# Performance work log

Hardware: AMD Instinct MI355X
Metric: run time of the kernel (lower is better)

Reference implementation:

```python
import jax, jax.numpy as jnp
import numpy as np

N_NODES = 100_000
N_EDGES = 3_200_000
D_IN, D_EDGE, D_HID, D_OUT = 8, 4, 32, 16
NEG_SLOPE = 0.2  # PyG GATv2Conv default


def setup_inputs() -> dict:
    key = jax.random.key(0)
    ks = jax.random.split(key, 13)
    s = 0.1
    return {
        "x": jax.random.normal(ks[0], (N_NODES, D_IN), jnp.float32),
        "edge_index": jax.random.randint(ks[1], (2, N_EDGES), 0, N_NODES, dtype=jnp.int64),
        "edge_attr": jax.random.normal(ks[2], (N_EDGES, D_EDGE), jnp.float32),
        "Wl1": jax.random.normal(ks[3], (D_IN, D_HID), jnp.float32) * s,
        "Wr1": jax.random.normal(ks[4], (D_IN, D_HID), jnp.float32) * s,
        "We1": jax.random.normal(ks[5], (D_EDGE, D_HID), jnp.float32) * s,
        "att1": jax.random.normal(ks[6], (D_HID,), jnp.float32) * s,
        "b1": jnp.zeros((D_HID,), jnp.float32),
        "Wl2": jax.random.normal(ks[7], (D_HID, D_OUT), jnp.float32) * s,
        "Wr2": jax.random.normal(ks[8], (D_HID, D_OUT), jnp.float32) * s,
        "We2": jax.random.normal(ks[9], (D_EDGE, D_OUT), jnp.float32) * s,
        "att2": jax.random.normal(ks[10], (D_OUT,), jnp.float32) * s,
        "b2": jnp.zeros((D_OUT,), jnp.float32),
    }


def _segment_softmax(score, seg, n):
    m = jax.ops.segment_max(score, seg, num_segments=n)
    e = jnp.exp(score - m[seg])
    z = jax.ops.segment_sum(e, seg, num_segments=n)
    return e / z[seg]


def _gatv2(x, src, dst, ea_raw, Wl, Wr, We, att, bias, n):
    # GATv2 (heads=1): score_ij = att . leaky_relu(Wl x_j + Wr x_i + We e_ij)
    xl = x @ Wl            # [N, d]
    xr = x @ Wr            # [N, d]
    ea = ea_raw @ We       # [E, d]
    h = jax.nn.leaky_relu(xl[src] + xr[dst] + ea, NEG_SLOPE)  # [E, d]
    score = h @ att        # [E]
    alpha = _segment_softmax(score, dst, n)
    out = jax.ops.segment_sum(alpha[:, None] * xl[src], dst, num_segments=n)
    return out + bias


def reference(x, edge_index, edge_attr, Wl1, Wr1, We1, att1, b1, Wl2, Wr2, We2, att2, b2):
    n = x.shape[0]
    src, dst = edge_index[0], edge_index[1]
    # add_self_loops=True with fill_value='mean': self-loop edge_attr = mean of
    # incoming raw edge_attr per target node (0 for isolated targets)
    ones = jnp.ones((src.shape[0],), x.dtype)
    cnt = jax.ops.segment_sum(ones, dst, num_segments=n)
    loop_attr = jax.ops.segment_sum(edge_attr, dst, num_segments=n) / jnp.maximum(cnt, 1.0)[:, None]
    ar = jnp.arange(n, dtype=src.dtype)
    src2 = jnp.concatenate([src, ar])
    dst2 = jnp.concatenate([dst, ar])
    ea2 = jnp.concatenate([edge_attr, loop_attr], axis=0)
    h = jax.nn.relu(_gatv2(x, src2, dst2, ea2, Wl1, Wr1, We1, att1, b1, n))
    out = _gatv2(h, src2, dst2, ea2, Wl2, Wr2, We2, att2, b2, n)
    return out.reshape(-1)
```

## Files before the change

kernel.cpp:

```cpp
#include <hip/hip_runtime.h>

#define NEG_SLOPE 0.2f
#define CHUNK 4096
#define KMAX  512
#define NBLKMAX 1024

__global__ __launch_bounds__(1024) void k_bin(const int* __restrict__ ei,
                                              const float* __restrict__ eattr,
                                              int* __restrict__ cloff,
                                              int* __restrict__ ssrc,
                                              float4* __restrict__ seat,
                                              int E, int K) {
    __shared__ int s_off[KMAX + 1];
    __shared__ int s_scan[1024];
    __shared__ int s_ssrc[CHUNK];
    __shared__ float4 s_seat[CHUNK];
    int t = threadIdx.x;
    for (int i = t; i <= K; i += 1024) s_off[i] = 0;
    __syncthreads();
    int base = blockIdx.x * CHUNK;
    int Ec = min(CHUNK, E - base);
    unsigned pack[CHUNK / 1024];
#pragma unroll
    for (int i = 0; i < CHUNK / 1024; i++) {
        int el = t + 1024 * i;
        pack[i] = 0xFFFFFFFFu;
        if (el < Ec) {
            int dst = ei[E + base + el];
            int b = dst >> 8;
            int r = atomicAdd(&s_off[b], 1);
            pack[i] = ((unsigned)b << 20) | ((unsigned)(dst & 255) << 12) | (unsigned)r;
        }
    }
    __syncthreads();
    int x0 = (t <= K) ? s_off[t] : 0;
    s_scan[t] = x0;
    __syncthreads();
    for (int off = 1; off < 1024; off <<= 1) {
        int y = (t >= off) ? s_scan[t - off] : 0;
        __syncthreads();
        s_scan[t] += y;
        __syncthreads();
    }
    if (t <= K) s_off[t] = s_scan[t] - x0;
    __syncthreads();
#pragma unroll
    for (int i = 0; i < CHUNK / 1024; i++) {
        int el = t + 1024 * i;
        if (el < Ec) {
            unsigned p = pack[i];
            int b = p >> 20;
            int dl = (p >> 12) & 255;
            int r = p & 0xFFF;
            int pos = s_off[b] + r;
            int e = base + el;
            s_ssrc[pos] = ei[e] | (dl << 17);
            s_seat[pos] = *(const float4*)(eattr + 4ll * e);
        }
    }
    __syncthreads();
    for (int pos = t; pos < Ec; pos += 1024) {
        ssrc[base + pos] = s_ssrc[pos];
        seat[base + pos] = s_seat[pos];
    }
    for (int i = t; i <= K; i += 1024)
        cloff[(long long)blockIdx.x * (K + 1) + i] = s_off[i];
}

__global__ void k_transp(const int* __restrict__ in, int* __restrict__ out, int R, int C) {
    __shared__ int tile[32][33];
    int c0 = blockIdx.x * 32, r0 = blockIdx.y * 32;
    int c = c0 + threadIdx.x, r = r0 + threadIdx.y;
    if (r < R && c < C) tile[threadIdx.y][threadIdx.x] = in[(long long)r * C + c];
    __syncthreads();
    int oc = r0 + threadIdx.x, orr = c0 + threadIdx.y;
    if (orr < C && oc < R) out[(long long)orr * R + oc] = tile[threadIdx.x][threadIdx.y];
}

__global__ void k_btot(const int* __restrict__ cloffT, int* __restrict__ bucketTotal,
                       int K, int NBLK) {
    int b = (blockIdx.x * blockDim.x + threadIdx.x) >> 6;
    int lane = threadIdx.x & 63;
    if (b >= K) return;
    const int* r0 = cloffT + (long long)b * NBLK;
    const int* r1 = r0 + NBLK;
    int s = 0;
    for (int c = lane; c < NBLK; c += 64) s += r1[c] - r0[c];
#pragma unroll
    for (int off = 32; off >= 1; off >>= 1) s += __shfl_xor(s, off, 64);
    if (lane == 0) bucketTotal[b] = s;
}

__global__ void k_scanK(const int* __restrict__ bucketTotal, int* __restrict__ slotBase,
                        int* __restrict__ qofs, int N, int K) {
    __shared__ int s[512];
    int t = threadIdx.x;
    int v[4];
    int sum = 0;
    int base = t * 4;
    for (int j = 0; j < 4; j++) {
        int b = base + j, x = 0;
        if (b < K) { int nb = min(256, N - (b << 8)); x = bucketTotal[b] + nb; }
        v[j] = sum;
        sum += x;
    }
    s[t] = sum;
    __syncthreads();
    for (int off = 1; off < 512; off <<= 1) {
        int x = (t >= off) ? s[t - off] : 0;
        __syncthreads();
        s[t] += x;
        __syncthreads();
    }
    int tb = s[t] - sum;
    for (int j = 0; j < 4; j++) {
        int b = base + j;
        if (b < K) slotBase[b] = tb + v[j];
    }
    if (t == 511) { slotBase[K] = s[511]; qofs[4ll * N] = s[511]; }
}

__global__ __launch_bounds__(1024, 2) void k_perm(const int* __restrict__ ssrc,
                                                  const float4* __restrict__ seat,
                                                  const int* __restrict__ cloffT,
                                                  const int* __restrict__ slotBase,
                                                  int* __restrict__ qofs,
                                                  int* __restrict__ fsrc,
                                                  float4* __restrict__ feat,
                                                  int N, int K, int NBLK, int QDIV) {
    __shared__ int co[NBLKMAX], qq[NBLKMAX + 1], sc[NBLKMAX];
    __shared__ int hist2[1024], cur2[1024], lst2[1024], sc2[1024];
    __shared__ int hist[256];
    __shared__ float lsum[256][4];
    int b = blockIdx.x, t = threadIdx.x;
    int nb = min(256, N - (b << 8));
    hist2[t] = 0; cur2[t] = 0;
    if (t < 256) { lsum[t][0] = 0.f; lsum[t][1] = 0.f; lsum[t][2] = 0.f; lsum[t][3] = 0.f; }
    const int* r0 = cloffT + (long long)b * NBLK;
    const int* r1 = r0 + NBLK;
    int len = 0;
    if (t < NBLK) { int c0v = r0[t]; len = r1[t] - c0v; co[t] = c0v; }
    sc[t] = (t < NBLK) ? len : 0;
    __syncthreads();
    for (int off = 1; off < NBLKMAX; off <<= 1) {
        int x = (t >= off) ? sc[t - off] : 0;
        __syncthreads();
        sc[t] += x;
        __syncthreads();
    }
    if (t < NBLK) qq[t] = sc[t] - len;
    if (t == NBLKMAX - 1) qq[NBLK] = sc[NBLKMAX - 1];
    __syncthreads();
    int Eb = qq[NBLK];
    for (int i = t; i < Eb; i += 1024) {
        int lo2 = 0, hi2 = NBLK;
        while (lo2 + 1 < hi2) { int mid = (lo2 + hi2) >> 1; if (qq[mid] <= i) lo2 = mid; else hi2 = mid; }
        int g = lo2 * CHUNK + co[lo2] + (i - qq[lo2]);
        int p = ssrc[g];
        int q = (int)((unsigned)(p & 0x1FFFF) / (unsigned)QDIV);
        atomicAdd(&hist2[(((p >> 17) & 255) << 2) | q], 1);
    }
    __syncthreads();
    if (t < 256) {
        int c = hist2[4 * t] + hist2[4 * t + 1] + hist2[4 * t + 2] + hist2[4 * t + 3];
        hist[t] = c;
        if (t < nb) {
            int node = (b << 8) + t;
            int qs = (int)((unsigned)node / (unsigned)QDIV);
            hist2[4 * t + qs] += 1;
            cur2[4 * t + qs] = 1;
        }
    }
    __syncthreads();
    sc2[t] = hist2[t];
    __syncthreads();
    for (int off = 1; off < 1024; off <<= 1) {
        int x = (t >= off) ? sc2[t - off] : 0;
        __syncthreads();
        sc2[t] += x;
        __syncthreads();
    }
    lst2[t] = sc2[t] - hist2[t];
    __syncthreads();
    int lo = slotBase[b];
    if (t < 4 * nb) qofs[((long long)b << 10) + t] = lo + lst2[t];
    for (int i = t; i < Eb; i += 1024) {
        int lo2 = 0, hi2 = NBLK;
        while (lo2 + 1 < hi2) { int mid = (lo2 + hi2) >> 1; if (qq[mid] <= i) lo2 = mid; else hi2 = mid; }
        int g = lo2 * CHUNK + co[lo2] + (i - qq[lo2]);
        int p = ssrc[g];
        int srcv = p & 0x1FFFF;
        int dl = (p >> 17) & 255;
        int q = (int)((unsigned)srcv / (unsigned)QDIV);
        int bin = (dl << 2) | q;
        int r = atomicAdd(&cur2[bin], 1);
        float4 a = seat[g];
        long long pos = lo + lst2[bin] + r;
        fsrc[pos] = srcv;
        feat[pos] = a;
        atomicAdd(&lsum[dl][0], a.x);
        atomicAdd(&lsum[dl][1], a.y);
        atomicAdd(&lsum[dl][2], a.z);
        atomicAdd(&lsum[dl][3], a.w);
    }
    __syncthreads();
    if (t < nb) {
        int node = (b << 8) + t;
        int qs = (int)((unsigned)node / (unsigned)QDIV);
        float inv = 1.f / fmaxf((float)hist[t], 1.f);
        long long pos = lo + lst2[4 * t + qs];
        fsrc[pos] = node;
        feat[pos] = make_float4(lsum[t][0] * inv, lsum[t][1] * inv,
                                lsum[t][2] * inv, lsum[t][3] * inv);
    }
}

template <int DIN, int D>
__global__ void k_xform(const float* __restrict__ x, const float* __restrict__ Wl,
                        const float* __restrict__ Wr, float* __restrict__ xl,
                        float* __restrict__ xr, int N) {
    __shared__ float sWl[DIN * D], sWr[DIN * D];
    for (int i = threadIdx.x; i < DIN * D; i += blockDim.x) { sWl[i] = Wl[i]; sWr[i] = Wr[i]; }
    __syncthreads();
    int t = blockIdx.x * blockDim.x + threadIdx.x;
    if (t >= N * D) return;
    int n = t / D, d = t % D;
    const float* xp = x + (long long)n * DIN;
    float sl = 0.f, sr = 0.f;
#pragma unroll
    for (int k = 0; k < DIN; k++) {
        float xv = xp[k];
        sl += xv * sWl[k * D + d];
        sr += xv * sWr[k * D + d];
    }
    xl[t] = sl;
    xr[t] = sr;
}

template <int L>
__device__ __forceinline__ void gat_edge(bool valid, const float4& a, const float4& xlv,
                                         const float4& we0, const float4& we1,
                                         const float4& we2, const float4& we3,
                                         const float4& av, const float4& xrv,
                                         float4& acc, float& z) {
    float4 v;
    v.x = fmaf(a.x, we0.x, xrv.x); v.x = fmaf(a.y, we1.x, v.x);
    v.x = fmaf(a.z, we2.x, v.x);   v.x = fmaf(a.w, we3.x, v.x); v.x += xlv.x;
    v.y = fmaf(a.x, we0.y, xrv.y); v.y = fmaf(a.y, we1.y, v.y);
    v.y = fmaf(a.z, we2.y, v.y);   v.y = fmaf(a.w, we3.y, v.y); v.y += xlv.y;
    v.z = fmaf(a.x, we0.z, xrv.z); v.z = fmaf(a.y, we1.z, v.z);
    v.z = fmaf(a.z, we2.z, v.z);   v.z = fmaf(a.w, we3.z, v.z); v.z += xlv.z;
    v.w = fmaf(a.x, we0.w, xrv.w); v.w = fmaf(a.y, we1.w, v.w);
    v.w = fmaf(a.z, we2.w, v.w);   v.w = fmaf(a.w, we3.w, v.w); v.w += xlv.w;
    v.x = v.x > 0.f ? v.x : NEG_SLOPE * v.x;
    v.y = v.y > 0.f ? v.y : NEG_SLOPE * v.y;
    v.z = v.z > 0.f ? v.z : NEG_SLOPE * v.z;
    v.w = v.w > 0.f ? v.w : NEG_SLOPE * v.w;
    float sc = av.x * v.x + av.y * v.y + av.z * v.z + av.w * v.w;
#pragma unroll
    for (int off = L / 2; off >= 1; off >>= 1) sc += __shfl_xor(sc, off, 64);
    float ev = valid ? __expf(sc) : 0.f;
    z += ev;
    acc.x = fmaf(ev, xlv.x, acc.x);
    acc.y = fmaf(ev, xlv.y, acc.y);
    acc.z = fmaf(ev, xlv.z, acc.z);
    acc.w = fmaf(ev, xlv.w, acc.w);
}

template <int D, bool RELU>
__global__ void k_gat(const int* __restrict__ fsrc,
                      const float4* __restrict__ feat,
                      const int* __restrict__ qofs,
                      const float* __restrict__ xl, const float* __restrict__ xr,
                      const float* __restrict__ We, const float* __restrict__ att,
                      const float* __restrict__ bias, float* __restrict__ out, int N) {
    constexpr int L = D / 4;
    constexpr int G = 64 / L;
    int w = (blockIdx.x * blockDim.x + threadIdx.x) >> 6;
    int lane = threadIdx.x & 63;
    if (w >= N) return;
    int g = lane / L;
    int j = lane % L;
    int s0 = qofs[4 * w], s1 = qofs[4 * w + 4];
    int cnt = s1 - s0;

    const float4 we0 = *(const float4*)(We + 0 * D + 4 * j);
    const float4 we1 = *(const float4*)(We + 1 * D + 4 * j);
    const float4 we2 = *(const float4*)(We + 2 * D + 4 * j);
    const float4 we3 = *(const float4*)(We + 3 * D + 4 * j);
    const float4 av  = *(const float4*)(att + 4 * j);
    const float4 xrv = *(const float4*)(xr + (long long)w * D + 4 * j);

    float4 acc = make_float4(0.f, 0.f, 0.f, 0.f);
    float z = 0.f;

    int it = 0;
    for (; (it + 2) * G <= cnt; it += 2) {
        int sl = s0 + it * G + g;
        int srcA = fsrc[sl];
        int srcB = fsrc[sl + G];
        float4 aA = feat[sl];
        float4 aB = feat[sl + G];
        float4 xA = *(const float4*)(xl + (long long)srcA * D + 4 * j);
        float4 xB = *(const float4*)(xl + (long long)srcB * D + 4 * j);
        gat_edge<L>(true, aA, xA, we0, we1, we2, we3, av, xrv, acc, z);
        gat_edge<L>(true, aB, xB, we0, we1, we2, we3, av, xrv, acc, z);
    }
    for (; it * G < cnt; ++it) {
        int o = it * G + g;
        bool v = o < cnt;
        int sl = s0 + min(o, cnt - 1);
        int src = fsrc[sl];
        float4 a = feat[sl];
        float4 xv = *(const float4*)(xl + (long long)src * D + 4 * j);
        gat_edge<L>(v, a, xv, we0, we1, we2, we3, av, xrv, acc, z);
    }

#pragma unroll
    for (int off = 32; off >= L; off >>= 1) {
        acc.x += __shfl_xor(acc.x, off, 64);
        acc.y += __shfl_xor(acc.y, off, 64);
        acc.z += __shfl_xor(acc.z, off, 64);
        acc.w += __shfl_xor(acc.w, off, 64);
        z += __shfl_xor(z, off, 64);
    }

    if (g == 0) {
        float inv = 1.0f / z;
        float4 bv = *(const float4*)(bias + 4 * j);
        float4 o;
        o.x = acc.x * inv + bv.x;
        o.y = acc.y * inv + bv.y;
        o.z = acc.z * inv + bv.z;
        o.w = acc.w * inv + bv.w;
        if (RELU) {
            o.x = fmaxf(o.x, 0.f); o.y = fmaxf(o.y, 0.f);
            o.z = fmaxf(o.z, 0.f); o.w = fmaxf(o.w, 0.f);
        }
        *(float4*)(out + (long long)w * D + 4 * j) = o;
    }
}

extern "C" void kernel_launch(void* const* d_in, const int* in_sizes, int n_in,
                              void* d_out, int out_size, void* d_ws, size_t ws_size,
                              hipStream_t stream) {
    const float* x     = (const float*)d_in[0];
    const int*   ei    = (const int*)d_in[1];
    const float* eattr = (const float*)d_in[2];
    const float* Wl1   = (const float*)d_in[3];
    const float* Wr1   = (const float*)d_in[4];
    const float* We1   = (const float*)d_in[5];
    const float* att1  = (const float*)d_in[6];
    const float* b1    = (const float*)d_in[7];
    const float* Wl2   = (const float*)d_in[8];
    const float* Wr2   = (const float*)d_in[9];
    const float* We2   = (const float*)d_in[10];
    const float* att2  = (const float*)d_in[11];
    const float* b2    = (const float*)d_in[12];

    const int N = in_sizes[0] / 8;
    const int E = in_sizes[1] / 2;
    const int K = (N + 255) >> 8;
    const int NBLK = (E + CHUNK - 1) / CHUNK;
    const int QDIV = (N + 3) / 4;

    int* iws = (int*)d_ws;
    size_t o = 0;
    int* bucketTotal = iws + o; o += K;
    int* slotBase    = iws + o; o += K + 1;
    int* qofs        = iws + o; o += 4ll * N + 1;
    int* cloff       = iws + o; o += (size_t)NBLK * (K + 1);
    int* cloffT      = iws + o; o += (size_t)(K + 1) * NBLK;
    o = (o + 7) & ~(size_t)7;
    int*    fsrc = (int*)(iws + o);    o += (size_t)(E + N);
    o = (o + 3) & ~(size_t)3;
    float4* feat = (float4*)(iws + o); o += 4ll * (E + N);
    size_t stage = o;
    int*    ssrc = (int*)(iws + o);    o += (size_t)E;
    o = (o + 3) & ~(size_t)3;
    float4* seat = (float4*)(iws + o); o += 4ll * E;
    float* xl = (float*)(iws + stage);
    float* xr = xl + 32ll * N;
    float* h  = xr + 32ll * N;

    const int B = 256;
    auto cdiv = [](long long a, long long b) { return (int)((a + b - 1) / b); };

    k_bin<<<NBLK, 1024, 0, stream>>>(ei, eattr, cloff, ssrc, seat, E, K);
    dim3 tb(32, 32);
    k_transp<<<dim3(cdiv(K + 1, 32), cdiv(NBLK, 32)), tb, 0, stream>>>(cloff, cloffT, NBLK, K + 1);
    k_btot<<<cdiv(64ll * K, B), B, 0, stream>>>(cloffT, bucketTotal, K, NBLK);
    k_scanK<<<1, 512, 0, stream>>>(bucketTotal, slotBase, qofs, N, K);
    k_perm<<<K, 1024, 0, stream>>>(ssrc, seat, cloffT, slotBase, qofs, fsrc, feat, N, K, NBLK, QDIV);

    k_xform<8, 32><<<cdiv(32ll * N, B), B, 0, stream>>>(x, Wl1, Wr1, xl, xr, N);
    k_gat<32, true><<<cdiv(N, 4), B, 0, stream>>>(fsrc, feat, qofs, xl, xr, We1, att1, b1, h, N);

    k_xform<32, 16><<<cdiv(16ll * N, B), B, 0, stream>>>(h, Wl2, Wr2, xl, xr, N);
    k_gat<16, false><<<cdiv(N, 4), B, 0, stream>>>(fsrc, feat, qofs, xl, xr, We2, att2, b2, (float*)d_out, N);
}
```

Before: 458.2 us.

## Cache packed keys in LDS and build inverse permutation for coalesced scatter writes

The permutation kernel now caches each edge's packed key in shared memory during the histogram pass, so the second pass no longer reloads it from global memory. The second pass only computes slot ranks and writes an inverse permutation into shared memory. A third pass then walks output positions in order, which makes the writes to fsrc and feat coalesced, while the edge-attribute reads become gathers. This uses about 74KB more LDS and drops to one block per CU, and blocks with more than CAPB edges would overflow the buffer.

```diff
diff --git a/kernel.cpp b/kernel.cpp
--- a/kernel.cpp
+++ b/kernel.cpp
@@ -4,6 +4,7 @@
 #define CHUNK 4096
 #define KMAX  512
 #define NBLKMAX 1024
+#define CAPB  9472
 
 __global__ __launch_bounds__(1024) void k_bin(const int* __restrict__ ei,
                                               const float* __restrict__ eattr,
@@ -120,7 +121,7 @@
     if (t == 511) { slotBase[K] = s[511]; qofs[4ll * N] = s[511]; }
 }
 
-__global__ __launch_bounds__(1024, 2) void k_perm(const int* __restrict__ ssrc,
+__global__ __launch_bounds__(1024, 1) void k_perm(const int* __restrict__ ssrc,
                                                   const float4* __restrict__ seat,
                                                   const int* __restrict__ cloffT,
                                                   const int* __restrict__ slotBase,
@@ -132,6 +133,8 @@
     __shared__ int hist2[1024], cur2[1024], lst2[1024], sc2[1024];
     __shared__ int hist[256];
     __shared__ float lsum[256][4];
+    __shared__ int s_p[CAPB];
+    __shared__ int s_inv[CAPB];
     int b = blockIdx.x, t = threadIdx.x;
     int nb = min(256, N - (b << 8));
     hist2[t] = 0; cur2[t] = 0;
@@ -157,6 +160,7 @@
         while (lo2 + 1 < hi2) { int mid = (lo2 + hi2) >> 1; if (qq[mid] <= i) lo2 = mid; else hi2 = mid; }
         int g = lo2 * CHUNK + co[lo2] + (i - qq[lo2]);
         int p = ssrc[g];
+        s_p[i] = p;
         int q = (int)((unsigned)(p & 0x1FFFF) / (unsigned)QDIV);
         atomicAdd(&hist2[(((p >> 17) & 255) << 2) | q], 1);
     }
@@ -184,24 +188,38 @@
     __syncthreads();
     int lo = slotBase[b];
     if (t < 4 * nb) qofs[((long long)b << 10) + t] = lo + lst2[t];
+    if (t < nb) {
+        int node = (b << 8) + t;
+        int qs = (int)((unsigned)node / (unsigned)QDIV);
+        s_inv[lst2[4 * t + qs]] = -(t + 1);
+    }
+    __syncthreads();
     for (int i = t; i < Eb; i += 1024) {
-        int lo2 = 0, hi2 = NBLK;
-        while (lo2 + 1 < hi2) { int mid = (lo2 + hi2) >> 1; if (qq[mid] <= i) lo2 = mid; else hi2 = mid; }
-        int g = lo2 * CHUNK + co[lo2] + (i - qq[lo2]);
-        int p = ssrc[g];
-        int srcv = p & 0x1FFFF;
-        int dl = (p >> 17) & 255;
-        int q = (int)((unsigned)srcv / (unsigned)QDIV);
-        int bin = (dl << 2) | q;
+        int p = s_p[i];
+        int q = (int)((unsigned)(p & 0x1FFFF) / (unsigned)QDIV);
+        int bin = (((p >> 17) & 255) << 2) | q;
         int r = atomicAdd(&cur2[bin], 1);
-        float4 a = seat[g];
-        long long pos = lo + lst2[bin] + r;
-        fsrc[pos] = srcv;
-        feat[pos] = a;
-        atomicAdd(&lsum[dl][0], a.x);
-        atomicAdd(&lsum[dl][1], a.y);
-        atomicAdd(&lsum[dl][2], a.z);
-        atomicAdd(&lsum[dl][3], a.w);
+        s_inv[lst2[bin] + r] = i;
+    }
+    __syncthreads();
+    int tot = Eb + nb;
+    for (int pos = t; pos < tot; pos += 1024) {
+        int i2 = s_inv[pos];
+        if (i2 >= 0) {
+            int p = s_p[i2];
+            int lo2 = 0, hi2 = NBLK;
+            while (lo2 + 1 < hi2) { int mid = (lo2 + hi2) >> 1; if (qq[mid] <= i2) lo2 = mid; else hi2 = mid; }
+            int g = lo2 * CHUNK + co[lo2] + (i2 - qq[lo2]);
+            float4 a = seat[g];
+            long long gp = lo + pos;
+            fsrc[gp] = p & 0x1FFFF;
+            feat[gp] = a;
+            int dl = (p >> 17) & 255;
+            atomicAdd(&lsum[dl][0], a.x);
+            atomicAdd(&lsum[dl][1], a.y);
+            atomicAdd(&lsum[dl][2], a.z);
+            atomicAdd(&lsum[dl][3], a.w);
+        }
     }
     __syncthreads();
     if (t < nb) {
```

Result: slower. 499.7 us (+9.1%).
